# Performance work log

Measured on AMD Instinct MI355X. Metric: run time of the kernel, lower is better.

## Reference

```python
import jax, jax.numpy as jnp
import numpy as np

B, S, D, H = 4, 2048, 768, 12
HD = D // H  # head_dim = 64

def setup_inputs() -> dict:
    key = jax.random.key(0)
    k1, k2, k3 = jax.random.split(key, 3)
    scale = 0.02
    return {
        "x": jax.random.normal(k1, (B, S, D), dtype=jnp.float32),
        "w_qkv": jax.random.normal(k2, (D, 3 * D), dtype=jnp.float32) * scale,
        "b_qkv": jnp.zeros((3 * D,), dtype=jnp.float32),
        "w_proj": jax.random.normal(k3, (D, D), dtype=jnp.float32) * scale,
        "b_proj": jnp.zeros((D,), dtype=jnp.float32),
    }

def reference(x, w_qkv, b_qkv, w_proj, b_proj):
    b, s, d = x.shape
    hd = d // H
    attn_scale = hd ** -0.5
    qkv = x @ w_qkv + b_qkv                      # [b, s, 3d]
    qkv = qkv.reshape(b, s, 3, H, hd)
    q, k, v = jnp.moveaxis(qkv, 2, 0)            # each [b, s, H, hd]
    q = q.transpose(0, 2, 1, 3)                  # [b, H, s, hd]
    k = k.transpose(0, 2, 1, 3)
    v = v.transpose(0, 2, 1, 3)
    attn = jnp.einsum("bhqd,bhkd->bhqk", q, k) * attn_scale  # [b, H, s, s]
    causal = jnp.tril(jnp.ones((s, s), dtype=bool))
    attn = jnp.where(causal[None, None], attn, -jnp.inf)
    attn = jax.nn.softmax(attn, axis=-1)
    out = jnp.einsum("bhqk,bhkd->bhqd", attn, v)  # [b, H, s, hd]
    out = out.transpose(0, 2, 1, 3).reshape(b, s, d)
    return out @ w_proj + b_proj
```

## Files before the change

kernel.cpp:

```cpp
#include <hip/hip_runtime.h>
#include <hip/hip_bf16.h>
#include <cstdint>

typedef __bf16 bf16_t;
typedef __bf16 bf16x4 __attribute__((ext_vector_type(4)));
typedef __bf16 bf16x8 __attribute__((ext_vector_type(8)));
typedef float floatx4 __attribute__((ext_vector_type(4)));
typedef float floatx16 __attribute__((ext_vector_type(16)));
typedef unsigned int u32x4 __attribute__((ext_vector_type(4)));

#define NB 4
#define NH 12
#define SEQ 2048
#define DM 768
#define LOG2E 1.44269504088896340736f

__device__ __forceinline__ void gload_lds16(const bf16_t* g, bf16_t* l) {
  auto gp = reinterpret_cast<const __attribute__((address_space(1))) uint32_t*>(
      reinterpret_cast<uintptr_t>(g));
  auto lp = reinterpret_cast<__attribute__((address_space(3))) uint32_t*>(
      reinterpret_cast<uintptr_t>(l));
  __builtin_amdgcn_global_load_lds(gp, lp, 16, 0, 0);
}

__device__ __forceinline__ unsigned int pack2(float a, float b) {
  bf16_t x = (bf16_t)a, y = (bf16_t)b;
  unsigned short ux = __builtin_bit_cast(unsigned short, x);
  unsigned short uy = __builtin_bit_cast(unsigned short, y);
  return (unsigned int)ux | ((unsigned int)uy << 16);
}

__global__ __launch_bounds__(256) void cvt_kernel(const float* __restrict__ in,
                                                  bf16_t* __restrict__ out) {
  int i = (blockIdx.x * 256 + threadIdx.x) * 4;
  float4 v = *(const float4*)(in + i);
  bf16x4 h;
  h[0] = (bf16_t)v.x; h[1] = (bf16_t)v.y; h[2] = (bf16_t)v.z; h[3] = (bf16_t)v.w;
  *(bf16x4*)(out + i) = h;
}

__global__ __launch_bounds__(256) void transpose_cvt_kernel(const float* __restrict__ in,
                                                            bf16_t* __restrict__ out,
                                                            int K, int N) {
  __shared__ float tile[32][33];
  int nb = blockIdx.x * 32, kb = blockIdx.y * 32;
  int tx = threadIdx.x & 31, ty = threadIdx.x >> 5;
#pragma unroll
  for (int r = ty; r < 32; r += 8)
    tile[r][tx] = in[(size_t)(kb + r) * N + nb + tx];
  __syncthreads();
#pragma unroll
  for (int r = ty; r < 32; r += 8)
    out[(size_t)(nb + r) * K + kb + tx] = (bf16_t)tile[tx][r];
}

__global__ __launch_bounds__(256) void gemm_qkv_kernel(
    const bf16_t* __restrict__ A, const bf16_t* __restrict__ BT,
    const float* __restrict__ bias,
    bf16_t* __restrict__ Qo, bf16_t* __restrict__ Ko, bf16_t* __restrict__ Vo) {
  const int K = 768;
  __shared__ __align__(16) bf16_t As[128][32];
  __shared__ __align__(16) bf16_t Bs[128][32];
  const int m0 = blockIdx.x * 128, n0 = blockIdx.y * 128;
  const int tid = threadIdx.x;
  const int w = tid >> 6, lane = tid & 63, quad = lane >> 4, l16 = lane & 15;
  const int wm = w >> 1, wn = w & 1;
  const int ldrow = w * 32;
  const int grow = lane >> 2;
  const int gcol = (lane & 3) * 8;

  floatx4 acc[4][4];
#pragma unroll
  for (int mt = 0; mt < 4; mt++)
#pragma unroll
    for (int nt = 0; nt < 4; nt++) acc[mt][nt] = (floatx4)(0.f);

  const bf16_t* ga0 = A + (size_t)(m0 + ldrow) * K;
  const bf16_t* gb0 = BT + (size_t)(n0 + ldrow) * K;

  for (int k0 = 0; k0 < K; k0 += 32) {
    __syncthreads();
    gload_lds16(ga0 + (size_t)grow * K + k0 + gcol,        &As[ldrow][0]);
    gload_lds16(ga0 + (size_t)(grow + 16) * K + k0 + gcol, &As[ldrow + 16][0]);
    gload_lds16(gb0 + (size_t)grow * K + k0 + gcol,        &Bs[ldrow][0]);
    gload_lds16(gb0 + (size_t)(grow + 16) * K + k0 + gcol, &Bs[ldrow + 16][0]);
    __syncthreads();
    bf16x8 af[4], bfr[4];
#pragma unroll
    for (int mt = 0; mt < 4; mt++)
      af[mt] = *(const bf16x8*)&As[wm * 64 + mt * 16 + l16][quad * 8];
#pragma unroll
    for (int nt = 0; nt < 4; nt++)
      bfr[nt] = *(const bf16x8*)&Bs[wn * 64 + nt * 16 + l16][quad * 8];
#pragma unroll
    for (int mt = 0; mt < 4; mt++)
#pragma unroll
      for (int nt = 0; nt < 4; nt++)
        acc[mt][nt] = __builtin_amdgcn_mfma_f32_16x16x32_bf16(af[mt], bfr[nt], acc[mt][nt], 0, 0, 0);
  }

  const int which = n0 / 768;
  const int rem0 = n0 % 768;
  bf16_t* dst = which == 0 ? Qo : (which == 1 ? Ko : Vo);
  const float qscale = which == 0 ? (0.125f * LOG2E) : 1.0f;
#pragma unroll
  for (int nt = 0; nt < 4; nt++) {
    const int cc = wn * 64 + nt * 16 + l16;
    const int rem = rem0 + cc;
    const int h = rem >> 6, hd = rem & 63;
    const float bv = bias[n0 + cc];
#pragma unroll
    for (int mt = 0; mt < 4; mt++)
#pragma unroll
      for (int r = 0; r < 4; r++) {
        const int gr = m0 + wm * 64 + mt * 16 + quad * 4 + r;
        const int bb = gr >> 11, s = gr & 2047;
        const float val = (acc[mt][nt][r] + bv) * qscale;
        dst[((size_t)((bb * NH + h) * SEQ + s)) * 64 + hd] = (bf16_t)val;
      }
  }
}

__global__ __launch_bounds__(256) void vtrans_kernel(const bf16_t* __restrict__ V,
                                                     bf16_t* __restrict__ Vt) {
  __shared__ bf16_t tile[64][66];
  int bh = blockIdx.y, s0 = blockIdx.x * 64;
  int tid = threadIdx.x;
  int r = tid >> 4, c4 = (tid & 15) * 4;
  const bf16_t* src = V + (size_t)bh * SEQ * 64;
#pragma unroll
  for (int rr = r; rr < 64; rr += 16)
    *(bf16x4*)&tile[rr][c4] = *(const bf16x4*)&src[(size_t)(s0 + rr) * 64 + c4];
  __syncthreads();
  bf16_t* dst = Vt + (size_t)bh * 64 * SEQ;
#pragma unroll
  for (int hd = r; hd < 64; hd += 16) {
    bf16x4 o;
    o[0] = tile[c4 + 0][hd]; o[1] = tile[c4 + 1][hd];
    o[2] = tile[c4 + 2][hd]; o[3] = tile[c4 + 3][hd];
    *(bf16x4*)&dst[(size_t)hd * SEQ + s0 + c4] = o;
  }
}

__global__ __launch_bounds__(256, 3) void attn_kernel(
    const bf16_t* __restrict__ Q, const bf16_t* __restrict__ Kg,
    const bf16_t* __restrict__ Vt, bf16_t* __restrict__ Out) {
  __shared__ __align__(16) bf16_t Ks[3][64 * 64];
  __shared__ __align__(16) bf16_t Vs[3][64 * 64];
  const int tid = threadIdx.x;
  const int w = tid >> 6, lane = tid & 63;
  const int l31 = lane & 31, hi = lane >> 5;
  const int bh = blockIdx.x;
  const int b = bh / NH, h = bh % NH;
  const int qt = (int)(gridDim.y - 1) - (int)blockIdx.y;
  const int r0 = qt * 128 + w * 32;
  const int qrow = r0 + l31;
  const bf16_t* Qp = Q + (size_t)bh * SEQ * 64;
  const bf16_t* Kp = Kg + (size_t)bh * SEQ * 64;
  const bf16_t* Vp = Vt + (size_t)bh * 64 * SEQ;

  bf16x8 qf[4];
#pragma unroll
  for (int kc = 0; kc < 4; kc++)
    qf[kc] = *(const bf16x8*)&Qp[(size_t)qrow * 64 + kc * 16 + hi * 8];

  float m_i = -1e30f, l_i = 0.f;
  floatx16 accT[2];
  accT[0] = (floatx16)(0.f);
  accT[1] = (floatx16)(0.f);

  const int nt_w = (r0 >> 6) + 1;
  const int ntmax = 2 * qt + 2;

  int srow[2], scolb[2];
#pragma unroll
  for (int r = 0; r < 2; r++) {
    int off = r * 4096 + w * 1024 + lane * 16;
    int row = off >> 7;
    srow[r] = row;
    scolb[r] = (off & 127) ^ ((row & 7) << 4);
  }

  auto stage = [&](int buf, int kt) {
    const int kbase = kt * 64;
#pragma unroll
    for (int r = 0; r < 2; r++) {
      gload_lds16(Kp + (size_t)(kbase + srow[r]) * 64 + (scolb[r] >> 1),
                  &Ks[buf][r * 2048 + w * 512]);
      gload_lds16(Vp + (size_t)srow[r] * SEQ + kbase + (scolb[r] >> 1),
                  &Vs[buf][r * 2048 + w * 512]);
    }
  };

  const int swz = (l31 & 7) << 4;

  stage(0, 0);

  int cur = 0;
  for (int kt = 0; kt < ntmax; kt++) {
    const int nxt = (cur == 2) ? 0 : cur + 1;
    if (kt + 1 < ntmax) {
      stage(nxt, kt + 1);
      asm volatile("s_waitcnt vmcnt(4)" ::: "memory");
    } else {
      asm volatile("s_waitcnt vmcnt(0)" ::: "memory");
    }
    __builtin_amdgcn_s_barrier();

    if (kt < nt_w) {
      const int kbase = kt * 64;
      const bf16_t* Kb = Ks[cur];
      const bf16_t* Vb = Vs[cur];
      floatx16 st[2];
#pragma unroll
      for (int kt2 = 0; kt2 < 2; kt2++) {
        const int row = kt2 * 32 + l31;
        floatx16 z = (floatx16)(0.f);
#pragma unroll
        for (int kc = 0; kc < 4; kc++) {
          bf16x8 kfr = *(const bf16x8*)&Kb[row * 64 + (((kc * 32 + hi * 16) ^ swz) >> 1)];
          z = __builtin_amdgcn_mfma_f32_32x32x16_bf16(kfr, qf[kc], z, 0, 0, 0);
        }
        st[kt2] = z;
      }
      if (kt == nt_w - 1) {
#pragma unroll
        for (int kt2 = 0; kt2 < 2; kt2++)
#pragma unroll
          for (int r = 0; r < 16; r++) {
            int key = kbase + kt2 * 32 + (r & 3) + 8 * (r >> 2) + 4 * hi;
            if (key > qrow) st[kt2][r] = -1e30f;
          }
      }
      float mloc = -1e30f;
#pragma unroll
      for (int kt2 = 0; kt2 < 2; kt2++)
#pragma unroll
        for (int r = 0; r < 16; r++) mloc = fmaxf(mloc, st[kt2][r]);
      mloc = fmaxf(mloc, __shfl_xor(mloc, 32));
      const float mnew = fmaxf(m_i, mloc);
      const float al = __builtin_amdgcn_exp2f(m_i - mnew);
      m_i = mnew;
      float ssum = 0.f;
#pragma unroll
      for (int kt2 = 0; kt2 < 2; kt2++)
#pragma unroll
        for (int r = 0; r < 16; r++) {
          float p = __builtin_amdgcn_exp2f(st[kt2][r] - mnew);
          st[kt2][r] = p;
          ssum += p;
        }
      ssum += __shfl_xor(ssum, 32);
      l_i = l_i * al + ssum;
#pragma unroll
      for (int dt = 0; dt < 2; dt++)
#pragma unroll
        for (int r = 0; r < 16; r++) accT[dt][r] *= al;
#pragma unroll
      for (int kt2 = 0; kt2 < 2; kt2++) {
        unsigned int wds[8];
#pragma unroll
        for (int j = 0; j < 8; j++) wds[j] = pack2(st[kt2][2 * j], st[kt2][2 * j + 1]);
        unsigned int x0 = (unsigned int)__shfl_xor((int)(hi ? wds[0] : wds[2]), 32);
        unsigned int x1 = (unsigned int)__shfl_xor((int)(hi ? wds[1] : wds[3]), 32);
        unsigned int x2 = (unsigned int)__shfl_xor((int)(hi ? wds[4] : wds[6]), 32);
        unsigned int x3 = (unsigned int)__shfl_xor((int)(hi ? wds[5] : wds[7]), 32);
        u32x4 f0 = hi ? (u32x4){x0, x1, wds[2], wds[3]} : (u32x4){wds[0], wds[1], x0, x1};
        u32x4 f1 = hi ? (u32x4){x2, x3, wds[6], wds[7]} : (u32x4){wds[4], wds[5], x2, x3};
        bf16x8 pf0 = __builtin_bit_cast(bf16x8, f0);
        bf16x8 pf1 = __builtin_bit_cast(bf16x8, f1);
#pragma unroll
        for (int dt = 0; dt < 2; dt++) {
          const int vrow = dt * 32 + l31;
          bf16x8 v0 = *(const bf16x8*)&Vb[vrow * 64 + (((kt2 * 64 + hi * 16) ^ swz) >> 1)];
          bf16x8 v1 = *(const bf16x8*)&Vb[vrow * 64 + (((kt2 * 64 + 32 + hi * 16) ^ swz) >> 1)];
          accT[dt] = __builtin_amdgcn_mfma_f32_32x32x16_bf16(v0, pf0, accT[dt], 0, 0, 0);
          accT[dt] = __builtin_amdgcn_mfma_f32_32x32x16_bf16(v1, pf1, accT[dt], 0, 0, 0);
        }
      }
    }
    cur = nxt;
  }

  const float inv_l = 1.0f / l_i;
#pragma unroll
  for (int dt = 0; dt < 2; dt++)
#pragma unroll
    for (int g = 0; g < 4; g++) {
      bf16x4 o;
#pragma unroll
      for (int j = 0; j < 4; j++) o[j] = (bf16_t)(accT[dt][4 * g + j] * inv_l);
      int d = dt * 32 + 8 * g + 4 * hi;
      *(bf16x4*)&Out[((size_t)(b * SEQ + qrow)) * DM + h * 64 + d] = o;
    }
}

__global__ __launch_bounds__(256) void gemm_proj_kernel(
    const bf16_t* __restrict__ A, const bf16_t* __restrict__ BT,
    const float* __restrict__ bias, float* __restrict__ out) {
  const int K = 768;
  __shared__ __align__(16) bf16_t As[128][32];
  __shared__ __align__(16) bf16_t Bs[128][32];
  const int m0 = blockIdx.x * 128, n0 = blockIdx.y * 128;
  const int tid = threadIdx.x;
  const int w = tid >> 6, lane = tid & 63, quad = lane >> 4, l16 = lane & 15;
  const int wm = w >> 1, wn = w & 1;
  const int ldrow = w * 32;
  const int grow = lane >> 2;
  const int gcol = (lane & 3) * 8;

  floatx4 acc[4][4];
#pragma unroll
  for (int mt = 0; mt < 4; mt++)
#pragma unroll
    for (int nt = 0; nt < 4; nt++) acc[mt][nt] = (floatx4)(0.f);

  const bf16_t* ga0 = A + (size_t)(m0 + ldrow) * K;
  const bf16_t* gb0 = BT + (size_t)(n0 + ldrow) * K;

  for (int k0 = 0; k0 < K; k0 += 32) {
    __syncthreads();
    gload_lds16(ga0 + (size_t)grow * K + k0 + gcol,        &As[ldrow][0]);
    gload_lds16(ga0 + (size_t)(grow + 16) * K + k0 + gcol, &As[ldrow + 16][0]);
    gload_lds16(gb0 + (size_t)grow * K + k0 + gcol,        &Bs[ldrow][0]);
    gload_lds16(gb0 + (size_t)(grow + 16) * K + k0 + gcol, &Bs[ldrow + 16][0]);
    __syncthreads();
    bf16x8 af[4], bfr[4];
#pragma unroll
    for (int mt = 0; mt < 4; mt++)
      af[mt] = *(const bf16x8*)&As[wm * 64 + mt * 16 + l16][quad * 8];
#pragma unroll
    for (int nt = 0; nt < 4; nt++)
      bfr[nt] = *(const bf16x8*)&Bs[wn * 64 + nt * 16 + l16][quad * 8];
#pragma unroll
    for (int mt = 0; mt < 4; mt++)
#pragma unroll
      for (int nt = 0; nt < 4; nt++)
        acc[mt][nt] = __builtin_amdgcn_mfma_f32_16x16x32_bf16(af[mt], bfr[nt], acc[mt][nt], 0, 0, 0);
  }

#pragma unroll
  for (int nt = 0; nt < 4; nt++) {
    const int gc = n0 + wn * 64 + nt * 16 + l16;
    const float bv = bias[gc];
#pragma unroll
    for (int mt = 0; mt < 4; mt++)
#pragma unroll
      for (int r = 0; r < 4; r++) {
        const int gr = m0 + wm * 64 + mt * 16 + quad * 4 + r;
        out[(size_t)gr * 768 + gc] = acc[mt][nt][r] + bv;
      }
  }
}

extern "C" void kernel_launch(void* const* d_in, const int* in_sizes, int n_in,
                              void* d_out, int out_size, void* d_ws, size_t ws_size,
                              hipStream_t stream) {
  const float* x      = (const float*)d_in[0];
  const float* w_qkv  = (const float*)d_in[1];
  const float* b_qkv  = (const float*)d_in[2];
  const float* w_proj = (const float*)d_in[3];
  const float* b_proj = (const float*)d_in[4];
  float* out = (float*)d_out;
  char* ws = (char*)d_ws;

  bf16_t* xb     = (bf16_t*)(ws + 0);
  bf16_t* wqkvT  = (bf16_t*)(ws + 12582912);
  bf16_t* wprojT = (bf16_t*)(ws + 16121856);
  bf16_t* q      = (bf16_t*)(ws + 17301504);
  bf16_t* k      = (bf16_t*)(ws + 29884416);
  bf16_t* v      = (bf16_t*)(ws + 42467328);
  bf16_t* ao     = (bf16_t*)(ws + 55050240);
  bf16_t* vt     = xb;

  cvt_kernel<<<6144, 256, 0, stream>>>(x, xb);
  transpose_cvt_kernel<<<dim3(72, 24), 256, 0, stream>>>(w_qkv, wqkvT, 768, 2304);
  transpose_cvt_kernel<<<dim3(24, 24), 256, 0, stream>>>(w_proj, wprojT, 768, 768);
  gemm_qkv_kernel<<<dim3(64, 18), 256, 0, stream>>>(xb, wqkvT, b_qkv, q, k, v);
  vtrans_kernel<<<dim3(32, 48), 256, 0, stream>>>(v, vt);
  attn_kernel<<<dim3(48, 16), 256, 0, stream>>>(q, k, vt, ao);
  gemm_proj_kernel<<<dim3(64, 6), 256, 0, stream>>>(ao, wprojT, b_proj, out);
}
```

Measured before the change: 208.8 us.

## Widen GEMM K-tile to 64 with XOR-swizzled LDS and add lazy softmax rescale

Both projection GEMMs now stage 64-wide K slices in LDS with an XOR swizzle on the column index. This halves the number of barrier pairs per tile and is meant to avoid LDS bank conflicts on the fragment reads. The attention loop skips the running-max update and the accumulator rescale unless some lane's new max exceeds the old one by more than 8 (in log2 units). The exponentials may then exceed 1 by up to 2^8, which is fine in fp32 but costs some bf16 precision in P. The GEMM change also doubles LDS use per block, which could lower occupancy.

```diff
diff --git a/kernel.cpp b/kernel.cpp
--- a/kernel.cpp
+++ b/kernel.cpp
@@ -59,15 +59,15 @@
     const float* __restrict__ bias,
     bf16_t* __restrict__ Qo, bf16_t* __restrict__ Ko, bf16_t* __restrict__ Vo) {
   const int K = 768;
-  __shared__ __align__(16) bf16_t As[128][32];
-  __shared__ __align__(16) bf16_t Bs[128][32];
+  __shared__ __align__(16) bf16_t As[128][64];
+  __shared__ __align__(16) bf16_t Bs[128][64];
   const int m0 = blockIdx.x * 128, n0 = blockIdx.y * 128;
   const int tid = threadIdx.x;
   const int w = tid >> 6, lane = tid & 63, quad = lane >> 4, l16 = lane & 15;
   const int wm = w >> 1, wn = w & 1;
-  const int ldrow = w * 32;
-  const int grow = lane >> 2;
-  const int gcol = (lane & 3) * 8;
+  const int sr = lane >> 3;
+  const int scol = ((lane & 7) ^ sr) * 8;
+  const int swzr = (l16 & 7) * 8;
 
   floatx4 acc[4][4];
 #pragma unroll
@@ -75,28 +75,30 @@
 #pragma unroll
     for (int nt = 0; nt < 4; nt++) acc[mt][nt] = (floatx4)(0.f);
 
-  const bf16_t* ga0 = A + (size_t)(m0 + ldrow) * K;
-  const bf16_t* gb0 = BT + (size_t)(n0 + ldrow) * K;
-
-  for (int k0 = 0; k0 < K; k0 += 32) {
+  for (int k0 = 0; k0 < K; k0 += 64) {
     __syncthreads();
-    gload_lds16(ga0 + (size_t)grow * K + k0 + gcol,        &As[ldrow][0]);
-    gload_lds16(ga0 + (size_t)(grow + 16) * K + k0 + gcol, &As[ldrow + 16][0]);
-    gload_lds16(gb0 + (size_t)grow * K + k0 + gcol,        &Bs[ldrow][0]);
-    gload_lds16(gb0 + (size_t)(grow + 16) * K + k0 + gcol, &Bs[ldrow + 16][0]);
+#pragma unroll
+    for (int r = 0; r < 4; r++) {
+      const int row = r * 32 + w * 8;
+      gload_lds16(A + (size_t)(m0 + row + sr) * K + k0 + scol, &As[row][0]);
+      gload_lds16(BT + (size_t)(n0 + row + sr) * K + k0 + scol, &Bs[row][0]);
+    }
     __syncthreads();
-    bf16x8 af[4], bfr[4];
-#pragma unroll
-    for (int mt = 0; mt < 4; mt++)
-      af[mt] = *(const bf16x8*)&As[wm * 64 + mt * 16 + l16][quad * 8];
-#pragma unroll
-    for (int nt = 0; nt < 4; nt++)
-      bfr[nt] = *(const bf16x8*)&Bs[wn * 64 + nt * 16 + l16][quad * 8];
-#pragma unroll
-    for (int mt = 0; mt < 4; mt++)
+#pragma unroll
+    for (int kk = 0; kk < 2; kk++) {
+      bf16x8 af[4], bfr[4];
+#pragma unroll
+      for (int mt = 0; mt < 4; mt++)
+        af[mt] = *(const bf16x8*)&As[wm * 64 + mt * 16 + l16][(kk * 32 + quad * 8) ^ swzr];
 #pragma unroll
       for (int nt = 0; nt < 4; nt++)
-        acc[mt][nt] = __builtin_amdgcn_mfma_f32_16x16x32_bf16(af[mt], bfr[nt], acc[mt][nt], 0, 0, 0);
+        bfr[nt] = *(const bf16x8*)&Bs[wn * 64 + nt * 16 + l16][(kk * 32 + quad * 8) ^ swzr];
+#pragma unroll
+      for (int mt = 0; mt < 4; mt++)
+#pragma unroll
+        for (int nt = 0; nt < 4; nt++)
+          acc[mt][nt] = __builtin_amdgcn_mfma_f32_16x16x32_bf16(af[mt], bfr[nt], acc[mt][nt], 0, 0, 0);
+    }
   }
 
   const int which = n0 / 768;
@@ -238,24 +240,27 @@
 #pragma unroll
         for (int r = 0; r < 16; r++) mloc = fmaxf(mloc, st[kt2][r]);
       mloc = fmaxf(mloc, __shfl_xor(mloc, 32));
-      const float mnew = fmaxf(m_i, mloc);
-      const float al = __builtin_amdgcn_exp2f(m_i - mnew);
-      m_i = mnew;
+      if (!__all((int)(mloc - m_i <= 8.f))) {
+        const float mnew = fmaxf(m_i, mloc);
+        const float al = __builtin_amdgcn_exp2f(m_i - mnew);
+        m_i = mnew;
+        l_i *= al;
+#pragma unroll
+        for (int dt = 0; dt < 2; dt++)
+#pragma unroll
+          for (int r = 0; r < 16; r++) accT[dt][r] *= al;
+      }
       float ssum = 0.f;
 #pragma unroll
       for (int kt2 = 0; kt2 < 2; kt2++)
 #pragma unroll
         for (int r = 0; r < 16; r++) {
-          float p = __builtin_amdgcn_exp2f(st[kt2][r] - mnew);
+          float p = __builtin_amdgcn_exp2f(st[kt2][r] - m_i);
           st[kt2][r] = p;
           ssum += p;
         }
       ssum += __shfl_xor(ssum, 32);
-      l_i = l_i * al + ssum;
-#pragma unroll
-      for (int dt = 0; dt < 2; dt++)
-#pragma unroll
-        for (int r = 0; r < 16; r++) accT[dt][r] *= al;
+      l_i += ssum;
 #pragma unroll
       for (int kt2 = 0; kt2 < 2; kt2++) {
         unsigned int wds[8];
@@ -299,15 +304,15 @@
     const bf16_t* __restrict__ A, const bf16_t* __restrict__ BT,
     const float* __restrict__ bias, float* __restrict__ out) {
   const int K = 768;
-  __shared__ __align__(16) bf16_t As[128][32];
-  __shared__ __align__(16) bf16_t Bs[128][32];
+  __shared__ __align__(16) bf16_t As[128][64];
+  __shared__ __align__(16) bf16_t Bs[128][64];
   const int m0 = blockIdx.x * 128, n0 = blockIdx.y * 128;
   const int tid = threadIdx.x;
   const int w = tid >> 6, lane = tid & 63, quad = lane >> 4, l16 = lane & 15;
   const int wm = w >> 1, wn = w & 1;
-  const int ldrow = w * 32;
-  const int grow = lane >> 2;
-  const int gcol = (lane & 3) * 8;
+  const int sr = lane >> 3;
+  const int scol = ((lane & 7) ^ sr) * 8;
+  const int swzr = (l16 & 7) * 8;
 
   floatx4 acc[4][4];
 #pragma unroll
@@ -315,28 +320,30 @@
 #pragma unroll
     for (int nt = 0; nt < 4; nt++) acc[mt][nt] = (floatx4)(0.f);
 
-  const bf16_t* ga0 = A + (size_t)(m0 + ldrow) * K;
-  const bf16_t* gb0 = BT + (size_t)(n0 + ldrow) * K;
-
-  for (int k0 = 0; k0 < K; k0 += 32) {
+  for (int k0 = 0; k0 < K; k0 += 64) {
     __syncthreads();
-    gload_lds16(ga0 + (size_t)grow * K + k0 + gcol,        &As[ldrow][0]);
-    gload_lds16(ga0 + (size_t)(grow + 16) * K + k0 + gcol, &As[ldrow + 16][0]);
-    gload_lds16(gb0 + (size_t)grow * K + k0 + gcol,        &Bs[ldrow][0]);
-    gload_lds16(gb0 + (size_t)(grow + 16) * K + k0 + gcol, &Bs[ldrow + 16][0]);
+#pragma unroll
+    for (int r = 0; r < 4; r++) {
+      const int row = r * 32 + w * 8;
+      gload_lds16(A + (size_t)(m0 + row + sr) * K + k0 + scol, &As[row][0]);
+      gload_lds16(BT + (size_t)(n0 + row + sr) * K + k0 + scol, &Bs[row][0]);
+    }
     __syncthreads();
-    bf16x8 af[4], bfr[4];
-#pragma unroll
-    for (int mt = 0; mt < 4; mt++)
-      af[mt] = *(const bf16x8*)&As[wm * 64 + mt * 16 + l16][quad * 8];
-#pragma unroll
-    for (int nt = 0; nt < 4; nt++)
-      bfr[nt] = *(const bf16x8*)&Bs[wn * 64 + nt * 16 + l16][quad * 8];
-#pragma unroll
-    for (int mt = 0; mt < 4; mt++)
+#pragma unroll
+    for (int kk = 0; kk < 2; kk++) {
+      bf16x8 af[4], bfr[4];
+#pragma unroll
+      for (int mt = 0; mt < 4; mt++)
+        af[mt] = *(const bf16x8*)&As[wm * 64 + mt * 16 + l16][(kk * 32 + quad * 8) ^ swzr];
 #pragma unroll
       for (int nt = 0; nt < 4; nt++)
-        acc[mt][nt] = __builtin_amdgcn_mfma_f32_16x16x32_bf16(af[mt], bfr[nt], acc[mt][nt], 0, 0, 0);
+        bfr[nt] = *(const bf16x8*)&Bs[wn * 64 + nt * 16 + l16][(kk * 32 + quad * 8) ^ swzr];
+#pragma unroll
+      for (int mt = 0; mt < 4; mt++)
+#pragma unroll
+        for (int nt = 0; nt < 4; nt++)
+          acc[mt][nt] = __builtin_amdgcn_mfma_f32_16x16x32_bf16(af[mt], bfr[nt], acc[mt][nt], 0, 0, 0);
+    }
   }
 
 #pragma unroll
```

Measured after the change: 214.9 us. 2.9% more time.
